# Kernel tuning notes

Measured on AMD Instinct MI355X. Metric: run time of the kernel, lower is better.

## Reference

```python
import jax, jax.numpy as jnp
import numpy as np

B, H, N, L = 8, 128, 64, 8192
LOG_DT_MIN, LOG_DT_MAX = float(np.log(0.001)), float(np.log(0.1))


def setup_inputs() -> dict:
    key = jax.random.key(0)
    k_x, k_are, k_aim, k_c, k_dt = jax.random.split(key, 5)
    x = jax.random.normal(k_x, (B, H, L), dtype=jnp.float32)
    # A_re: negative real parts (clipped to <= -1e-4 in forward anyway)
    A_re = -jax.random.uniform(k_are, (H, N, 1), dtype=jnp.float32, minval=0.1, maxval=1.0)
    A_im = jax.random.normal(k_aim, (H, N, 1), dtype=jnp.float32) * float(np.pi)
    C = (0.5 ** 0.5) * jax.random.normal(k_c, (H, N, 2), dtype=jnp.float32)
    D = jnp.ones((1, H, 1), dtype=jnp.float32)
    u = jax.random.uniform(k_dt, (H, 1, 1), dtype=jnp.float32)
    log_delta = u * (LOG_DT_MAX - LOG_DT_MIN) + LOG_DT_MIN
    return {"x": x, "A_re": A_re, "A_im": A_im, "C": C, "D": D, "log_delta": log_delta}


def reference(x, A_re, A_im, C, D, log_delta):
    seq_len = x.shape[-1]
    # ---- S4D-ZOH kernel generation ----
    A = jnp.minimum(A_re, -1e-4) + 1j * A_im            # (H, N, 1) complex
    Cc = C[..., 0:1] + 1j * C[..., 1:2]                 # (H, N, 1) complex
    step = jnp.exp(log_delta)                           # (H, 1, 1)
    dA = step * A                                       # (H, N, 1)
    times = jnp.arange(seq_len, dtype=jnp.float32)[None, None, :]  # (1, 1, L)
    part = jnp.exp(times * dA)                          # (H, N, L)
    cons = (jnp.exp(dA) - 1.0) / A                      # (H, N, 1)
    K = jnp.sum(Cc * cons * part, axis=-2).real         # (H, L)
    # ---- causal conv via FFT (torch pads both to length 2L) ----
    n = seq_len + K.shape[-1]                           # 2L
    xd = jnp.fft.rfft(x, n=n, axis=-1)                  # (B, H, L+1)
    Kd = jnp.fft.rfft(K[None], n=n, axis=-1)            # (1, H, L+1)
    conv = jnp.fft.irfft(xd * Kd, n=n, axis=-1)[:, :, :seq_len]
    return conv + D * x
```

## Files before the change

### kernel.cpp

```cpp
#include <hip/hip_runtime.h>
#include <math.h>

#define B_ 8
#define H_ 128
#define N_ 64
#define L_ 8192
#define MCH 64
#define SCH (L_ / MCH)
#define EROW 136

typedef __attribute__((ext_vector_type(8))) short bf16x8;
typedef __attribute__((ext_vector_type(4))) float f32x4;

__device__ __forceinline__ ushort f2bf(float f) {
    uint u = __float_as_uint(f);
    return (ushort)((u + 0x7fffu + ((u >> 16) & 1u)) >> 16);
}
__device__ __forceinline__ float bf2f(ushort s) { return __uint_as_float(((uint)s) << 16); }
__device__ __forceinline__ uint packbf2(float a, float b) {
    return (uint)f2bf(a) | ((uint)f2bf(b) << 16);
}
__device__ __forceinline__ bf16x8 pack_bf8(float4 a, float4 b) {
    bf16x8 r;
    r[0] = (short)f2bf(a.x); r[1] = (short)f2bf(a.y); r[2] = (short)f2bf(a.z); r[3] = (short)f2bf(a.w);
    r[4] = (short)f2bf(b.x); r[5] = (short)f2bf(b.y); r[6] = (short)f2bf(b.z); r[7] = (short)f2bf(b.w);
    return r;
}

__global__ __launch_bounds__(64) void s4d_build(
    const float* __restrict__ A_re, const float* __restrict__ A_im,
    const float* __restrict__ C, const float* __restrict__ D,
    const float* __restrict__ log_delta,
    ushort* __restrict__ wsT, ushort* __restrict__ wsP,
    ushort* __restrict__ wsQ, float2* __restrict__ wsRM)
{
    __shared__ float cbuf[64 * 65];
    __shared__ float kv[64];
    __shared__ uint  pbuf[64 * 68];

    const int h = blockIdx.x, n = threadIdx.x;

    float are = fminf(A_re[h * N_ + n], -1e-4f);
    float aim = A_im[h * N_ + n];
    float step = expf(log_delta[h]);
    float dre = step * are, dim = step * aim;
    float er = expf(dre);
    float rr = er * cosf(dim);
    float ri = er * sinf(dim);
    float cre = C[(h * N_ + n) * 2 + 0];
    float cim = C[(h * N_ + n) * 2 + 1];
    float inv  = 1.0f / (are * are + aim * aim);
    float numr = rr - 1.0f, numi = ri;
    float consr = (numr * are + numi * aim) * inv;
    float consi = (numi * are - numr * aim) * inv;
    float wr = cre * consr - cim * consi;
    float wi = cre * consi + cim * consr;
    float dval = D[h];

    float mr = rr, mi = ri;
#pragma unroll
    for (int k = 0; k < 6; ++k) { float tr = mr*mr - mi*mi, ti = 2.f*mr*mi; mr = tr; mi = ti; }
    wsRM[h * 64 + n] = make_float2(mr, mi);

    float pr = wr, pi = wi;
#pragma unroll
    for (int d = 0; d < 64; ++d) {
        cbuf[n * 65 + d] = pr;
        float tr = pr*rr - pi*ri, ti = pr*ri + pi*rr;
        pr = tr; pi = ti;
    }
    __syncthreads();
    float ks = 0.f;
#pragma unroll
    for (int m = 0; m < 64; ++m) ks += cbuf[m * 65 + n];
    kv[n] = ks;
    __syncthreads();

    uint trow[32];
#pragma unroll
    for (int t = 0; t < 64; t += 2) {
        float v0 = (t     <= n) ? kv[n - t]     : 0.f;
        float v1 = (t + 1 <= n) ? kv[n - t - 1] : 0.f;
        if (t == n)     v0 += dval;
        if (t + 1 == n) v1 += dval;
        trow[t >> 1] = packbf2(v0, v1);
    }
    uint4* dT = (uint4*)(wsT + ((size_t)h * 64 + n) * 64);
#pragma unroll
    for (int i = 0; i < 8; ++i) dT[i] = ((uint4*)trow)[i];

    union { ushort u[64]; uint4 v4[8]; } qre, qim;
    float ppr = 1.f, ppi = 0.f;
#pragma unroll
    for (int i = 0; i < 64; ++i) {
        qre.u[63 - i] = f2bf(ppr);
        qim.u[63 - i] = f2bf(ppi);
        float tr = ppr*rr - ppi*ri, ti = ppr*ri + ppi*rr;
        ppr = tr; ppi = ti;
    }
    uint4* dQ0 = (uint4*)(wsQ + ((size_t)h * 128 + 2*n    ) * 64);
    uint4* dQ1 = (uint4*)(wsQ + ((size_t)h * 128 + 2*n + 1) * 64);
#pragma unroll
    for (int i = 0; i < 8; ++i) { dQ0[i] = qre.v4[i]; dQ1[i] = qim.v4[i]; }

    float uur = wr*rr - wi*ri, uui = wr*ri + wi*rr;
#pragma unroll
    for (int j = 0; j < 64; ++j) {
        pbuf[j * 68 + n] = packbf2(uur, -uui);
        float tr = uur*rr - uui*ri, ti = uur*ri + uui*rr;
        uur = tr; uui = ti;
    }
    __syncthreads();
    uint4* dP = (uint4*)(wsP + ((size_t)h * 64 + n) * 128);
#pragma unroll
    for (int i = 0; i < 16; ++i) dP[i] = *(const uint4*)&pbuf[n * 68 + i * 4];
}

__global__ __launch_bounds__(256) void s4d_main(
    const float* __restrict__ x,
    const ushort* __restrict__ wsT, const ushort* __restrict__ wsP,
    const ushort* __restrict__ wsQ, const float2* __restrict__ wsRM,
    float* __restrict__ out)
{
    __shared__ ushort EBUF[SCH * EROW];

    const int seq = blockIdx.x;
    const int h   = seq % H_;
    const int tid = threadIdx.x;
    const int w   = tid >> 6;
    const int lane = tid & 63;
    const int n16 = lane & 15, q = lane >> 4;

    const float* xs = x + (size_t)seq * L_;

    bf16x8 xb[2][2];
#pragma unroll
    for (int ic = 0; ic < 2; ++ic) {
        int c = (2 * w + ic) * 16 + n16;
#pragma unroll
        for (int kc = 0; kc < 2; ++kc) {
            const float* p = xs + c * MCH + kc * 32 + q * 8;
            float4 f0 = *(const float4*)p;
            float4 f1 = *(const float4*)(p + 4);
            xb[ic][kc] = pack_bf8(f0, f1);
        }
    }

    const ushort* Qh = wsQ + (size_t)h * 128 * 64;
#pragma unroll
    for (int ic = 0; ic < 2; ++ic) {
        int c = (2 * w + ic) * 16 + n16;
#pragma unroll
        for (int rt = 0; rt < 8; ++rt) {
            f32x4 acc = {0.f, 0.f, 0.f, 0.f};
#pragma unroll
            for (int kc = 0; kc < 2; ++kc) {
                bf16x8 a = *(const bf16x8*)(Qh + ((size_t)(rt * 16 + n16)) * 64 + kc * 32 + q * 8);
                acc = __builtin_amdgcn_mfma_f32_16x16x32_bf16(a, xb[ic][kc], acc, 0, 0, 0);
            }
            ushort4 st;
            st.x = f2bf(acc[0]); st.y = f2bf(acc[1]); st.z = f2bf(acc[2]); st.w = f2bf(acc[3]);
            *(ushort4*)&EBUF[c * EROW + rt * 16 + q * 4] = st;
        }
    }
    __syncthreads();

    if (tid < 64) {
        float2 rm = wsRM[h * 64 + tid];
        float sr = 0.f, si = 0.f;
        for (int c = 0; c < SCH; ++c) {
            uint* ep = (uint*)&EBUF[c * EROW + 2 * tid];
            uint e = *ep;
            float er2 = bf2f((ushort)(e & 0xffffu));
            float ei2 = bf2f((ushort)(e >> 16));
            *ep = packbf2(sr, si);
            float nr = er2 + rm.x * sr - rm.y * si;
            float ni = ei2 + rm.x * si + rm.y * sr;
            sr = nr; si = ni;
        }
    }
    __syncthreads();

    const ushort* Th = wsT + (size_t)h * 64 * 64;
    const ushort* Ph = wsP + (size_t)h * 64 * 128;
    float* op = out + (size_t)seq * L_;
#pragma unroll
    for (int ic = 0; ic < 2; ++ic) {
        int c = (2 * w + ic) * 16 + n16;
        bf16x8 svb[4];
#pragma unroll
        for (int kc = 0; kc < 4; ++kc)
            svb[kc] = *(const bf16x8*)&EBUF[c * EROW + kc * 32 + q * 8];
#pragma unroll
        for (int rt = 0; rt < 4; ++rt) {
            f32x4 acc = {0.f, 0.f, 0.f, 0.f};
#pragma unroll
            for (int kc = 0; kc < 2; ++kc) {
                bf16x8 a = *(const bf16x8*)(Th + ((size_t)(rt * 16 + n16)) * 64 + kc * 32 + q * 8);
                acc = __builtin_amdgcn_mfma_f32_16x16x32_bf16(a, xb[ic][kc], acc, 0, 0, 0);
            }
#pragma unroll
            for (int kc = 0; kc < 4; ++kc) {
                bf16x8 a = *(const bf16x8*)(Ph + ((size_t)(rt * 16 + n16)) * 128 + kc * 32 + q * 8);
                acc = __builtin_amdgcn_mfma_f32_16x16x32_bf16(a, svb[kc], acc, 0, 0, 0);
            }
            float4 o = make_float4(acc[0], acc[1], acc[2], acc[3]);
            *(float4*)(op + c * MCH + rt * 16 + q * 4) = o;
        }
    }
}

extern "C" void kernel_launch(void* const* d_in, const int* in_sizes, int n_in,
                              void* d_out, int out_size, void* d_ws, size_t ws_size,
                              hipStream_t stream)
{
    const float* x  = (const float*)d_in[0];
    const float* Ar = (const float*)d_in[1];
    const float* Ai = (const float*)d_in[2];
    const float* C  = (const float*)d_in[3];
    const float* D  = (const float*)d_in[4];
    const float* ld = (const float*)d_in[5];
    float* out = (float*)d_out;

    ushort* wsT = (ushort*)d_ws;
    ushort* wsP = wsT + (size_t)128 * 64 * 64;
    ushort* wsQ = wsP + (size_t)128 * 64 * 128;
    float2* wsRM = (float2*)(wsQ + (size_t)128 * 128 * 64);

    hipLaunchKernelGGL(s4d_build, dim3(H_), dim3(64), 0, stream,
                       Ar, Ai, C, D, ld, wsT, wsP, wsQ, wsRM);
    hipLaunchKernelGGL(s4d_main, dim3(B_ * H_), dim3(256), 0, stream,
                       x, wsT, wsP, wsQ, wsRM, out);
}
```

Before: 126.8 us.

## Parallelize S4D build and chunk scan across all warps, hoist MFMA operand loads

The build kernel now uses 256 threads and computes powers of the decay directly with exp/sincos instead of serial complex multiplication, so each of the four warps fills a quarter of the T, Q and P tables. In the main kernel, the 128-step sequential chunk-state scan that ran on one warp is split into four 32-chunk segments, with a second pass that combines segment carries using r^2048. MFMA A-operand loads are hoisted out of the inner loop so they are shared across the two column tiles, and launch bounds request four blocks per CU. The gain is more parallelism in the serial scan and build, at the cost of an extra barrier, more scan arithmetic, and slightly different rounding from the direct exponentials.

```diff
diff --git a/kernel.cpp b/kernel.cpp
--- a/kernel.cpp
+++ b/kernel.cpp
@@ -27,18 +27,21 @@
     return r;
 }
 
-__global__ __launch_bounds__(64) void s4d_build(
+__global__ __launch_bounds__(256) void s4d_build(
     const float* __restrict__ A_re, const float* __restrict__ A_im,
     const float* __restrict__ C, const float* __restrict__ D,
     const float* __restrict__ log_delta,
     ushort* __restrict__ wsT, ushort* __restrict__ wsP,
     ushort* __restrict__ wsQ, float2* __restrict__ wsRM)
 {
-    __shared__ float cbuf[64 * 65];
+    __shared__ float kpart[64][65];
     __shared__ float kv[64];
     __shared__ uint  pbuf[64 * 68];
 
-    const int h = blockIdx.x, n = threadIdx.x;
+    const int h = blockIdx.x;
+    const int tid = threadIdx.x;
+    const int n = tid & 63;
+    const int g = tid >> 6;
 
     float are = fminf(A_re[h * N_ + n], -1e-4f);
     float aim = A_im[h * N_ + n];
@@ -57,72 +60,90 @@
     float wi = cre * consi + cim * consr;
     float dval = D[h];
 
-    float mr = rr, mi = ri;
-#pragma unroll
-    for (int k = 0; k < 6; ++k) { float tr = mr*mr - mi*mi, ti = 2.f*mr*mi; mr = tr; mi = ti; }
-    wsRM[h * 64 + n] = make_float2(mr, mi);
-
-    float pr = wr, pi = wi;
-#pragma unroll
-    for (int d = 0; d < 64; ++d) {
-        cbuf[n * 65 + d] = pr;
-        float tr = pr*rr - pi*ri, ti = pr*ri + pi*rr;
-        pr = tr; pi = ti;
-    }
-    __syncthreads();
-    float ks = 0.f;
-#pragma unroll
-    for (int m = 0; m < 64; ++m) ks += cbuf[m * 65 + n];
-    kv[n] = ks;
-    __syncthreads();
-
-    uint trow[32];
-#pragma unroll
-    for (int t = 0; t < 64; t += 2) {
-        float v0 = (t     <= n) ? kv[n - t]     : 0.f;
-        float v1 = (t + 1 <= n) ? kv[n - t - 1] : 0.f;
-        if (t == n)     v0 += dval;
-        if (t + 1 == n) v1 += dval;
-        trow[t >> 1] = packbf2(v0, v1);
-    }
-    uint4* dT = (uint4*)(wsT + ((size_t)h * 64 + n) * 64);
-#pragma unroll
-    for (int i = 0; i < 8; ++i) dT[i] = ((uint4*)trow)[i];
-
-    union { ushort u[64]; uint4 v4[8]; } qre, qim;
-    float ppr = 1.f, ppi = 0.f;
-#pragma unroll
-    for (int i = 0; i < 64; ++i) {
-        qre.u[63 - i] = f2bf(ppr);
-        qim.u[63 - i] = f2bf(ppi);
-        float tr = ppr*rr - ppi*ri, ti = ppr*ri + ppi*rr;
-        ppr = tr; ppi = ti;
-    }
-    uint4* dQ0 = (uint4*)(wsQ + ((size_t)h * 128 + 2*n    ) * 64);
-    uint4* dQ1 = (uint4*)(wsQ + ((size_t)h * 128 + 2*n + 1) * 64);
-#pragma unroll
-    for (int i = 0; i < 8; ++i) { dQ0[i] = qre.v4[i]; dQ1[i] = qim.v4[i]; }
-
-    float uur = wr*rr - wi*ri, uui = wr*ri + wi*rr;
-#pragma unroll
-    for (int j = 0; j < 64; ++j) {
-        pbuf[j * 68 + n] = packbf2(uur, -uui);
-        float tr = uur*rr - uui*ri, ti = uur*ri + uui*rr;
-        uur = tr; uui = ti;
-    }
-    __syncthreads();
-    uint4* dP = (uint4*)(wsP + ((size_t)h * 64 + n) * 128);
-#pragma unroll
-    for (int i = 0; i < 16; ++i) dP[i] = *(const uint4*)&pbuf[n * 68 + i * 4];
-}
-
-__global__ __launch_bounds__(256) void s4d_main(
+    auto rp = [&](float d, float& pr, float& pi) {
+        float e = expf(d * dre);
+        float s, c2; sincosf(d * dim, &s, &c2);
+        pr = e * c2; pi = e * s;
+    };
+
+#pragma unroll
+    for (int j = 0; j < 16; ++j) {
+        int d = g * 16 + j;
+        float pr, pi; rp((float)d, pr, pi);
+        kpart[d][n] = wr * pr - wi * pi;
+    }
+    __syncthreads();
+    if (tid < 64) {
+        float s = 0.f;
+#pragma unroll
+        for (int m = 0; m < 64; ++m) s += kpart[tid][m];
+        kv[tid] = s;
+    }
+    __syncthreads();
+
+    {
+        uint tw[8];
+#pragma unroll
+        for (int i = 0; i < 8; ++i) {
+            int t0 = g * 16 + 2 * i, t1 = t0 + 1;
+            float v0 = (t0 <= n) ? kv[n - t0] : 0.f;
+            float v1 = (t1 <= n) ? kv[n - t1] : 0.f;
+            if (t0 == n) v0 += dval;
+            if (t1 == n) v1 += dval;
+            tw[i] = packbf2(v0, v1);
+        }
+        uint4* dT = (uint4*)(wsT + ((size_t)h * 64 + n) * 64 + g * 16);
+        dT[0] = ((uint4*)tw)[0]; dT[1] = ((uint4*)tw)[1];
+    }
+
+    {
+        uint qr[8], qi[8];
+#pragma unroll
+        for (int i = 0; i < 8; ++i) {
+            int t0 = g * 16 + 2 * i;
+            float ar0, ai0, ar1, ai1;
+            rp((float)(63 - t0), ar0, ai0);
+            rp((float)(62 - t0), ar1, ai1);
+            qr[i] = packbf2(ar0, ar1);
+            qi[i] = packbf2(ai0, ai1);
+        }
+        uint4* dQ0 = (uint4*)(wsQ + ((size_t)h * 128 + 2 * n    ) * 64 + g * 16);
+        uint4* dQ1 = (uint4*)(wsQ + ((size_t)h * 128 + 2 * n + 1) * 64 + g * 16);
+        dQ0[0] = ((uint4*)qr)[0]; dQ0[1] = ((uint4*)qr)[1];
+        dQ1[0] = ((uint4*)qi)[0]; dQ1[1] = ((uint4*)qi)[1];
+    }
+
+#pragma unroll
+    for (int i = 0; i < 16; ++i) {
+        int j = g * 16 + i;
+        float pr, pi; rp((float)(j + 1), pr, pi);
+        float ur = wr * pr - wi * pi;
+        float ui = wr * pi + wi * pr;
+        pbuf[j * 68 + n] = packbf2(ur, -ui);
+    }
+    if (tid < 64) {
+        float mr, mi; rp(64.f, mr, mi);
+        wsRM[h * 64 + n] = make_float2(mr, mi);
+    }
+    __syncthreads();
+    {
+        uint4* dP = (uint4*)(wsP + ((size_t)h * 64 + n) * 128 + g * 32);
+        const uint* src = &pbuf[n * 68 + g * 16];
+        dP[0] = *(const uint4*)(src);
+        dP[1] = *(const uint4*)(src + 4);
+        dP[2] = *(const uint4*)(src + 8);
+        dP[3] = *(const uint4*)(src + 12);
+    }
+}
+
+__global__ __launch_bounds__(256, 4) void s4d_main(
     const float* __restrict__ x,
     const ushort* __restrict__ wsT, const ushort* __restrict__ wsP,
     const ushort* __restrict__ wsQ, const float2* __restrict__ wsRM,
     float* __restrict__ out)
 {
     __shared__ ushort EBUF[SCH * EROW];
+    __shared__ float segr[4][64], segi[4][64];
 
     const int seq = blockIdx.x;
     const int h   = seq % H_;
@@ -148,16 +169,15 @@
 
     const ushort* Qh = wsQ + (size_t)h * 128 * 64;
 #pragma unroll
-    for (int ic = 0; ic < 2; ++ic) {
-        int c = (2 * w + ic) * 16 + n16;
-#pragma unroll
-        for (int rt = 0; rt < 8; ++rt) {
+    for (int rt = 0; rt < 8; ++rt) {
+        bf16x8 a0 = *(const bf16x8*)(Qh + ((size_t)(rt * 16 + n16)) * 64 +      q * 8);
+        bf16x8 a1 = *(const bf16x8*)(Qh + ((size_t)(rt * 16 + n16)) * 64 + 32 + q * 8);
+#pragma unroll
+        for (int ic = 0; ic < 2; ++ic) {
             f32x4 acc = {0.f, 0.f, 0.f, 0.f};
-#pragma unroll
-            for (int kc = 0; kc < 2; ++kc) {
-                bf16x8 a = *(const bf16x8*)(Qh + ((size_t)(rt * 16 + n16)) * 64 + kc * 32 + q * 8);
-                acc = __builtin_amdgcn_mfma_f32_16x16x32_bf16(a, xb[ic][kc], acc, 0, 0, 0);
-            }
+            acc = __builtin_amdgcn_mfma_f32_16x16x32_bf16(a0, xb[ic][0], acc, 0, 0, 0);
+            acc = __builtin_amdgcn_mfma_f32_16x16x32_bf16(a1, xb[ic][1], acc, 0, 0, 0);
+            int c = (2 * w + ic) * 16 + n16;
             ushort4 st;
             st.x = f2bf(acc[0]); st.y = f2bf(acc[1]); st.z = f2bf(acc[2]); st.w = f2bf(acc[3]);
             *(ushort4*)&EBUF[c * EROW + rt * 16 + q * 4] = st;
@@ -165,17 +185,43 @@
     }
     __syncthreads();
 
-    if (tid < 64) {
-        float2 rm = wsRM[h * 64 + tid];
+    {
+        const int nB = tid & 63, gB = tid >> 6;
+        float2 rm = wsRM[h * 64 + nB];
+        float mr = rm.x, mi = rm.y;
+        float m32r = mr, m32i = mi;
+#pragma unroll
+        for (int k = 0; k < 5; ++k) {
+            float tr = m32r * m32r - m32i * m32i, ti = 2.f * m32r * m32i;
+            m32r = tr; m32i = ti;
+        }
         float sr = 0.f, si = 0.f;
-        for (int c = 0; c < SCH; ++c) {
-            uint* ep = (uint*)&EBUF[c * EROW + 2 * tid];
+#pragma unroll
+        for (int j = 0; j < 32; ++j) {
+            uint e = *(const uint*)&EBUF[(gB * 32 + j) * EROW + 2 * nB];
+            float er2 = bf2f((ushort)(e & 0xffffu)), ei2 = bf2f((ushort)(e >> 16));
+            float nr = er2 + mr * sr - mi * si;
+            float ni = ei2 + mr * si + mi * sr;
+            sr = nr; si = ni;
+        }
+        segr[gB][nB] = sr; segi[gB][nB] = si;
+        __syncthreads();
+        float pr2 = 0.f, pi2 = 0.f;
+        for (int gp = 0; gp < gB; ++gp) {
+            float Er = segr[gp][nB], Ei = segi[gp][nB];
+            float nr = Er + m32r * pr2 - m32i * pi2;
+            float ni = Ei + m32r * pi2 + m32i * pr2;
+            pr2 = nr; pi2 = ni;
+        }
+        sr = pr2; si = pi2;
+#pragma unroll
+        for (int j = 0; j < 32; ++j) {
+            uint* ep = (uint*)&EBUF[(gB * 32 + j) * EROW + 2 * nB];
             uint e = *ep;
-            float er2 = bf2f((ushort)(e & 0xffffu));
-            float ei2 = bf2f((ushort)(e >> 16));
+            float er2 = bf2f((ushort)(e & 0xffffu)), ei2 = bf2f((ushort)(e >> 16));
             *ep = packbf2(sr, si);
-            float nr = er2 + rm.x * sr - rm.y * si;
-            float ni = ei2 + rm.x * si + rm.y * sr;
+            float nr = er2 + mr * sr - mi * si;
+            float ni = ei2 + mr * si + mi * sr;
             sr = nr; si = ni;
         }
     }
@@ -184,26 +230,33 @@
     const ushort* Th = wsT + (size_t)h * 64 * 64;
     const ushort* Ph = wsP + (size_t)h * 64 * 128;
     float* op = out + (size_t)seq * L_;
+
+    bf16x8 svb[2][4];
 #pragma unroll
     for (int ic = 0; ic < 2; ++ic) {
         int c = (2 * w + ic) * 16 + n16;
-        bf16x8 svb[4];
 #pragma unroll
         for (int kc = 0; kc < 4; ++kc)
-            svb[kc] = *(const bf16x8*)&EBUF[c * EROW + kc * 32 + q * 8];
-#pragma unroll
-        for (int rt = 0; rt < 4; ++rt) {
+            svb[ic][kc] = *(const bf16x8*)&EBUF[c * EROW + kc * 32 + q * 8];
+    }
+#pragma unroll
+    for (int rt = 0; rt < 4; ++rt) {
+        bf16x8 t0 = *(const bf16x8*)(Th + ((size_t)(rt * 16 + n16)) * 64 +      q * 8);
+        bf16x8 t1 = *(const bf16x8*)(Th + ((size_t)(rt * 16 + n16)) * 64 + 32 + q * 8);
+        bf16x8 p0 = *(const bf16x8*)(Ph + ((size_t)(rt * 16 + n16)) * 128 +       q * 8);
+        bf16x8 p1 = *(const bf16x8*)(Ph + ((size_t)(rt * 16 + n16)) * 128 +  32 + q * 8);
+        bf16x8 p2 = *(const bf16x8*)(Ph + ((size_t)(rt * 16 + n16)) * 128 +  64 + q * 8);
+        bf16x8 p3 = *(const bf16x8*)(Ph + ((size_t)(rt * 16 + n16)) * 128 +  96 + q * 8);
+#pragma unroll
+        for (int ic = 0; ic < 2; ++ic) {
             f32x4 acc = {0.f, 0.f, 0.f, 0.f};
-#pragma unroll
-            for (int kc = 0; kc < 2; ++kc) {
-                bf16x8 a = *(const bf16x8*)(Th + ((size_t)(rt * 16 + n16)) * 64 + kc * 32 + q * 8);
-                acc = __builtin_amdgcn_mfma_f32_16x16x32_bf16(a, xb[ic][kc], acc, 0, 0, 0);
-            }
-#pragma unroll
-            for (int kc = 0; kc < 4; ++kc) {
-                bf16x8 a = *(const bf16x8*)(Ph + ((size_t)(rt * 16 + n16)) * 128 + kc * 32 + q * 8);
-                acc = __builtin_amdgcn_mfma_f32_16x16x32_bf16(a, svb[kc], acc, 0, 0, 0);
-            }
+            acc = __builtin_amdgcn_mfma_f32_16x16x32_bf16(t0, xb[ic][0], acc, 0, 0, 0);
+            acc = __builtin_amdgcn_mfma_f32_16x16x32_bf16(t1, xb[ic][1], acc, 0, 0, 0);
+            acc = __builtin_amdgcn_mfma_f32_16x16x32_bf16(p0, svb[ic][0], acc, 0, 0, 0);
+            acc = __builtin_amdgcn_mfma_f32_16x16x32_bf16(p1, svb[ic][1], acc, 0, 0, 0);
+            acc = __builtin_amdgcn_mfma_f32_16x16x32_bf16(p2, svb[ic][2], acc, 0, 0, 0);
+            acc = __builtin_amdgcn_mfma_f32_16x16x32_bf16(p3, svb[ic][3], acc, 0, 0, 0);
+            int c = (2 * w + ic) * 16 + n16;
             float4 o = make_float4(acc[0], acc[1], acc[2], acc[3]);
             *(float4*)(op + c * MCH + rt * 16 + q * 4) = o;
         }
@@ -227,7 +280,7 @@
     ushort* wsQ = wsP + (size_t)128 * 64 * 128;
     float2* wsRM = (float2*)(wsQ + (size_t)128 * 128 * 64);
 
-    hipLaunchKernelGGL(s4d_build, dim3(H_), dim3(64), 0, stream,
+    hipLaunchKernelGGL(s4d_build, dim3(H_), dim3(256), 0, stream,
                        Ar, Ai, C, D, ld, wsT, wsP, wsQ, wsRM);
     hipLaunchKernelGGL(s4d_main, dim3(B_ * H_), dim3(256), 0, stream,
                        x, wsT, wsP, wsQ, wsRM, out);
```

Measured after the change: 122.6 us. 3.3% less time.
